# Optimization experiments

Hardware: AMD Instinct MI355X
Metric: run time of the kernel (lower is better)

## Reference

```python
import jax, jax.numpy as jnp
import numpy as np


def setup_inputs() -> dict:
    key = jax.random.key(0)
    k1, k2, k3 = jax.random.split(key, 3)
    B, S, D = 2, 2048, 1024
    N_COMPRESS, RANK = 64, 64
    x = jax.random.normal(k1, (B, S, D), dtype=jnp.float32)
    router_w = jax.random.normal(k2, (N_COMPRESS, D), dtype=jnp.float32) * (1.0 / np.sqrt(D))
    # compress neurons (orthogonal-init in torch; gaussian scaled is fine for a numeric baseline)
    neurons = jax.random.normal(k3, (N_COMPRESS, D, RANK), dtype=jnp.float32) * (1.0 / np.sqrt(D))
    return {"x": x, "router_w": router_w, "neurons": neurons}


TOP_K = 2


def reference(x, router_w, neurons):
    # x: [B,S,D], router_w: [N,D], neurons: [N,D,R]
    B, S, D = x.shape
    R = neurons.shape[-1]
    scores = jnp.einsum('bsd,nd->bsn', x, router_w)            # [B,S,N]
    topk_scores, topk_idx = jax.lax.top_k(scores, TOP_K)       # [B,S,K]
    topk_weights = jax.nn.softmax(topk_scores, axis=-1)        # [B,S,K]
    output = jnp.zeros((B, S, R), dtype=x.dtype)
    for i in range(TOP_K):  # small fixed loop, mirrors original slot-wise combine
        idx = topk_idx[:, :, i]                                # [B,S]
        sel = neurons[idx]                                     # [B,S,D,R] gather
        proj = jnp.einsum('bsd,bsdr->bsr', x, sel)             # per-token matvec
        output = output + topk_weights[:, :, i:i + 1] * proj
    return output, topk_idx, topk_weights
```

## Files before the change

### kernel.cpp

```cpp
#include <hip/hip_runtime.h>
#include <hip/hip_bf16.h>


typedef unsigned short u16;
typedef unsigned int u32;
typedef __attribute__((ext_vector_type(8))) short short8;
typedef __attribute__((ext_vector_type(4))) float f32x4;

__device__ __forceinline__ float bf2f(u16 u) {
    u32 v = ((u32)u) << 16; float f; __builtin_memcpy(&f, &v, 4); return f;
}
__device__ __forceinline__ u16 f2bf(float f) {
    u32 u; __builtin_memcpy(&u, &f, 4);
    u32 r = u + 0x7fff + ((u >> 16) & 1);
    return (u16)(r >> 16);
}
__device__ __forceinline__ u32 pack2(float a, float b) {
    return ((u32)f2bf(b) << 16) | (u32)f2bf(a);
}

#define T_TOKENS 4096
#define DDIM 1024
#define NEXP 64
#define RDIM 64
#define LCAP 1024
#define OUT_IDX_OFF 262144
#define OUT_W_OFF 270336

struct LdBF {
    const u16* p;
    __device__ __forceinline__ float4 ld4(size_t i) const {
        ushort4 v = *(const ushort4*)(p + i);
        return make_float4(bf2f(v.x), bf2f(v.y), bf2f(v.z), bf2f(v.w));
    }
    __device__ __forceinline__ float ld1(size_t i) const { return bf2f(p[i]); }
};
struct LdF32 {
    const float* p;
    __device__ __forceinline__ float4 ld4(size_t i) const { return *(const float4*)(p + i); }
    __device__ __forceinline__ float ld1(size_t i) const { return p[i]; }
};

__device__ __forceinline__ int detect_f32(const u16* x, int* lds_cnt) {
    if (threadIdx.x == 0) *lds_cnt = 0;
    __syncthreads();
    if (threadIdx.x < 256) {
        unsigned e = (x[threadIdx.x] >> 7) & 0xFF;
        if (e >= 0x68 && e <= 0x88) atomicAdd(lds_cnt, 1);
    }
    __syncthreads();
    int f = (*lds_cnt < 200) ? 1 : 0;
    __syncthreads();
    return f;
}

template <class LD>
__device__ __forceinline__ void score_body(LD xld, LD rwld,
                                           float* xs , float* wt ,
                                           float* sc , float* Sb) {
    const int tid = threadIdx.x;
    const int g = blockIdx.x >> 1;
    const int kh = blockIdx.x & 1;
    const size_t t0 = (size_t)g * 8;
    const int kbase = kh * 512;
    const int wv = tid >> 6;
    const int lane = tid & 63;
    const int tg = lane & 1;
    const int eg = (lane >> 1) & 7;
    const int kql = (lane >> 4) & 3;
    const int dd = 4 * kql + 16 * wv;
    const int kc0 = blockIdx.x & 7;

    const int sm = tid >> 4;
    const int sd4 = (tid & 15) * 4;

    float acc[4][8];
#pragma unroll
    for (int mi = 0; mi < 4; ++mi)
#pragma unroll
        for (int ei = 0; ei < 8; ++ei) acc[mi][ei] = 0.f;

    float4 px;
    if (tid < 128) px = xld.ld4((t0 + sm) * DDIM + kbase + kc0 * 64 + sd4);
    float4 pw[4];
#pragma unroll
    for (int h = 0; h < 4; ++h) {
        int i4 = tid + h * 256;
        pw[h] = rwld.ld4((size_t)(i4 >> 4) * DDIM + kbase + kc0 * 64 + (i4 & 15) * 4);
    }

    for (int i = 0; i < 8; ++i) {
        if (i > 0) __syncthreads();
        if (tid < 128) *(float4*)&xs[sm * 68 + sd4] = px;
#pragma unroll
        for (int h = 0; h < 4; ++h) {
            int i4 = tid + h * 256;
            *(float4*)&wt[(i4 >> 4) * 68 + (i4 & 15) * 4] = pw[h];
        }
        __syncthreads();

        if (i < 7) {
            int kn = kbase + ((i + 1 + kc0) & 7) * 64;
            if (tid < 128) px = xld.ld4((t0 + sm) * DDIM + kn + sd4);
#pragma unroll
            for (int h = 0; h < 4; ++h) {
                int i4 = tid + h * 256;
                pw[h] = rwld.ld4((size_t)(i4 >> 4) * DDIM + kn + (i4 & 15) * 4);
            }
        }

        float4 xv[4], wv4[8];
#pragma unroll
        for (int mi = 0; mi < 4; ++mi)
            xv[mi] = *(const float4*)&xs[(tg + 2 * mi) * 68 + dd];
#pragma unroll
        for (int ei = 0; ei < 8; ++ei)
            wv4[ei] = *(const float4*)&wt[(eg + 8 * ei) * 68 + dd];
#pragma unroll
        for (int mi = 0; mi < 4; ++mi)
#pragma unroll
            for (int ei = 0; ei < 8; ++ei)
                acc[mi][ei] += xv[mi].x * wv4[ei].x + xv[mi].y * wv4[ei].y +
                               xv[mi].z * wv4[ei].z + xv[mi].w * wv4[ei].w;
    }

#pragma unroll
    for (int mi = 0; mi < 4; ++mi)
#pragma unroll
        for (int ei = 0; ei < 8; ++ei) {
            float v = acc[mi][ei];
            v += __shfl_xor(v, 16, 64);
            v += __shfl_xor(v, 32, 64);
            acc[mi][ei] = v;
        }
    __syncthreads();

    for (int w = 0; w < 4; ++w) {
        if (wv == w && kql == 0) {
#pragma unroll
            for (int mi = 0; mi < 4; ++mi)
#pragma unroll
                for (int ei = 0; ei < 8; ++ei) {
                    int idx = (tg + 2 * mi) * 65 + eg + 8 * ei;
                    sc[idx] = (w == 0) ? acc[mi][ei] : sc[idx] + acc[mi][ei];
                }
        }
        __syncthreads();
    }

    if (tid < 128) {
        int t = tid >> 4, e4 = (tid & 15) * 4;
        const float* s = &sc[t * 65 + e4];
        float4 v = make_float4(s[0], s[1], s[2], s[3]);
        *(float4*)&Sb[((size_t)kh * T_TOKENS + t0 + t) * 64 + e4] = v;
    }
}

__global__ __launch_bounds__(256, 4) void score_part(const void* x, const void* rw,
                                                     float* Sb) {
    __shared__ float xs[8 * 68];
    __shared__ float wt[64 * 68];
    __shared__ float sc[8 * 65];
    __shared__ int dc;
    int f = detect_f32((const u16*)x, &dc);
    if (f)
        score_body(LdF32{(const float*)x}, LdF32{(const float*)rw}, xs, wt, sc, Sb);
    else
        score_body(LdBF{(const u16*)x}, LdBF{(const u16*)rw}, xs, wt, sc, Sb);
}

__global__ __launch_bounds__(64) void topk_softmax(const float* Sb, float* out,
                                                   float* wsW, int* wsCnt,
                                                   int* wsList) {
    int t = blockIdx.x * 64 + threadIdx.x;
    const float* s0 = Sb + (size_t)t * 64;
    const float* s1 = Sb + ((size_t)T_TOKENS + t) * 64;
    float best = -1e30f, secv = -1e30f;
    int bi = 0, si = 0;
    for (int j = 0; j < NEXP; j += 4) {
        float4 a = *(const float4*)(s0 + j);
        float4 b = *(const float4*)(s1 + j);
        float v0 = a.x + b.x, v1 = a.y + b.y, v2 = a.z + b.z, v3 = a.w + b.w;
        if (v0 > best) { secv = best; si = bi; best = v0; bi = j; }
        else if (v0 > secv) { secv = v0; si = j; }
        if (v1 > best) { secv = best; si = bi; best = v1; bi = j + 1; }
        else if (v1 > secv) { secv = v1; si = j + 1; }
        if (v2 > best) { secv = best; si = bi; best = v2; bi = j + 2; }
        else if (v2 > secv) { secv = v2; si = j + 2; }
        if (v3 > best) { secv = best; si = bi; best = v3; bi = j + 3; }
        else if (v3 > secv) { secv = v3; si = j + 3; }
    }
    float w0 = 1.0f / (1.0f + expf(secv - best));
    float w1 = 1.0f - w0;
    out[OUT_IDX_OFF + (size_t)t * 2 + 0] = (float)bi;
    out[OUT_IDX_OFF + (size_t)t * 2 + 1] = (float)si;
    out[OUT_W_OFF + (size_t)t * 2 + 0] = w0;
    out[OUT_W_OFF + (size_t)t * 2 + 1] = w1;
    wsW[t * 2 + 0] = w0;
    wsW[t * 2 + 1] = w1;
    int p0 = atomicAdd(&wsCnt[bi], 1);
    if (p0 < LCAP) wsList[bi * LCAP + p0] = t * 2 + 0;
    int p1 = atomicAdd(&wsCnt[si], 1);
    if (p1 < LCAP) wsList[si * LCAP + p1] = t * 2 + 1;
}

template <class LD>
__device__ __forceinline__ void egemm_body(LD xld, LD nld,
                                           const int* wsCnt, const int* wsList,
                                           float* P,
                                           u16* Ab , u16* Bb ,
                                           int* eL ) {
    const int tid = threadIdx.x;
    const int e = blockIdx.x >> 3;
    const int oct = blockIdx.x & 7;
    const int cntE = min(wsCnt[e], LCAP);
    if (cntE <= 0) return;
    const int wv = tid >> 6;
    const int lane = tid & 63;
    const int l15 = lane & 15, quad = lane >> 4;
    const size_t nbase = (size_t)e * (DDIM * RDIM);
    const int k0 = oct * 128;

    for (int j = tid; j < cntE; j += 256) eL[j] = wsList[e * LCAP + j];

    {
        const int rq = tid & 15;
        const int kpB = tid >> 4;
        u32* bb = (u32*)Bb;
#pragma unroll
        for (int h = 0; h < 4; ++h) {
            int kp = kpB + h * 16;
            float4 g0 = nld.ld4(nbase + (size_t)(k0 + 2 * kp) * RDIM + rq * 4);
            float4 g1 = nld.ld4(nbase + (size_t)(k0 + 2 * kp + 1) * RDIM + rq * 4);
            bb[(rq * 4 + 0) * 68 + kp] = pack2(g0.x, g1.x);
            bb[(rq * 4 + 1) * 68 + kp] = pack2(g0.y, g1.y);
            bb[(rq * 4 + 2) * 68 + kp] = pack2(g0.z, g1.z);
            bb[(rq * 4 + 3) * 68 + kp] = pack2(g0.w, g1.w);
        }
    }
    __syncthreads();

    const int rowA = tid >> 4;
    const int kqA = tid & 15;
    const int ntiles = (cntE + 15) >> 4;

    float4 c0, c1, n0, n1;
    {
        int t2r = eL[min(rowA, cntE - 1)];
        size_t xrow = (size_t)(t2r >> 1) * DDIM + k0;
        c0 = xld.ld4(xrow + kqA * 8);
        c1 = xld.ld4(xrow + kqA * 8 + 4);
    }
    n0 = c0; n1 = c1;
    if (ntiles > 1) {
        int t2r = eL[min(16 + rowA, cntE - 1)];
        size_t xrow = (size_t)(t2r >> 1) * DDIM + k0;
        n0 = xld.ld4(xrow + kqA * 8);
        n1 = xld.ld4(xrow + kqA * 8 + 4);
    }

    for (int ti = 0; ti < ntiles; ++ti) {
        const int base = ti * 16;
        const int valid = min(16, cntE - base);
        if (ti > 0) __syncthreads();
        {
            uint4 w;
            w.x = pack2(c0.x, c0.y);
            w.y = pack2(c0.z, c0.w);
            w.z = pack2(c1.x, c1.y);
            w.w = pack2(c1.z, c1.w);
            *(uint4*)&((u32*)Ab)[rowA * 68 + kqA * 4] = w;
        }
        __syncthreads();
        if (ti + 2 < ntiles) {
            int t2r = eL[min(base + 32 + rowA, cntE - 1)];
            size_t xrow = (size_t)(t2r >> 1) * DDIM + k0;
            c0 = xld.ld4(xrow + kqA * 8);
            c1 = xld.ld4(xrow + kqA * 8 + 4);
        }

        f32x4 acc = {0.f, 0.f, 0.f, 0.f};
#pragma unroll
        for (int ko = 0; ko < 4; ++ko) {
            int kofs = ko * 32 + quad * 8;
            short8 bfr = *(const short8*)&Bb[(16 * wv + l15) * 136 + kofs];
            short8 af = *(const short8*)&Ab[l15 * 136 + kofs];
            acc = __builtin_amdgcn_mfma_f32_16x16x32_bf16(af, bfr, acc, 0, 0, 0);
        }

#pragma unroll
        for (int reg = 0; reg < 4; ++reg) {
            int m = quad * 4 + reg;
            if (m < valid) {
                int t2 = eL[base + m];
                P[(size_t)t2 * 512 + oct * 64 + 16 * wv + l15] = acc[reg];
            }
        }

        float4 s0 = c0, s1 = c1;
        c0 = n0; c1 = n1;
        n0 = s0; n1 = s1;
    }
}

__global__ __launch_bounds__(256, 2) void expert_gemm(const void* x, const void* neurons,
                                                      const int* wsCnt, const int* wsList,
                                                      float* P) {
    __shared__ u16 Ab[16 * 136];
    __shared__ u16 Bb[64 * 136];
    __shared__ int eL[LCAP];
    __shared__ int dc;
    int f = detect_f32((const u16*)x, &dc);
    if (f)
        egemm_body(LdF32{(const float*)x}, LdF32{(const float*)neurons}, wsCnt, wsList, P, Ab, Bb, eL);
    else
        egemm_body(LdBF{(const u16*)x}, LdBF{(const u16*)neurons}, wsCnt, wsList, P, Ab, Bb, eL);
}

__global__ __launch_bounds__(256) void combine(const float* P, const float* wsW,
                                               float* out) {
    int i = blockIdx.x * 256 + threadIdx.x;
    int t = i >> 6, r = i & 63;
    const float* p0 = P + (size_t)(2 * t) * 512 + r;
    const float* p1 = P + (size_t)(2 * t + 1) * 512 + r;
    float s0 = 0.f, s1 = 0.f;
#pragma unroll
    for (int o = 0; o < 8; ++o) {
        s0 += p0[o * 64];
        s1 += p1[o * 64];
    }
    out[i] = wsW[2 * t] * s0 + wsW[2 * t + 1] * s1;
}

extern "C" void kernel_launch(void* const* d_in, const int* in_sizes, int n_in,
                              void* d_out, int out_size, void* d_ws, size_t ws_size,
                              hipStream_t stream) {
    const void* x = d_in[0];
    const void* rw = d_in[1];
    const void* neurons = d_in[2];
    float* out = (float*)d_out;

    char* wsc = (char*)d_ws;
    float* wsW = (float*)wsc;
    int* wsCnt = (int*)(wsc + 32 * 1024);
    int* wsList = (int*)(wsc + 32 * 1024 + 256);
    float* Sb = (float*)(wsc + (1 << 20));
    float* P = (float*)(wsc + (4 << 20));

    hipMemsetAsync(wsCnt, 0, 256, stream);
    score_part<<<1024, 256, 0, stream>>>(x, rw, Sb);
    topk_softmax<<<64, 64, 0, stream>>>(Sb, out, wsW, wsCnt, wsList);
    expert_gemm<<<512, 256, 0, stream>>>(x, neurons, wsCnt, wsList, P);
    combine<<<1024, 256, 0, stream>>>(P, wsW, out);
}
```

Measured before the change: 123.9 us.

## Keep router-weight K-slice resident in LDS and stream token tiles through it

The score kernel now splits K into four quarters per block and loads that 64x256 router-weight slice into LDS once. It then loops over eight 8-token tiles, prefetching the next tile of x, instead of reloading the full router tile for every 8 tokens. This removes the redundant router-weight global traffic, but the grid drops from 1024 to 256 blocks at one block per SM, and LDS use grows to about 80 KB. Partial scores now come in four K-quarters, so topk_softmax sums four buffers and the workspace offset for P moves to make room.

```diff
diff --git a/kernel.cpp b/kernel.cpp
--- a/kernel.cpp
+++ b/kernel.cpp
@@ -56,117 +56,130 @@
 
 template <class LD>
 __device__ __forceinline__ void score_body(LD xld, LD rwld,
-                                           float* xs , float* wt ,
-                                           float* sc , float* Sb) {
+                                           float* wt4 , float* xs4 ,
+                                           float* scW , float* Sb) {
     const int tid = threadIdx.x;
-    const int g = blockIdx.x >> 1;
-    const int kh = blockIdx.x & 1;
-    const size_t t0 = (size_t)g * 8;
-    const int kbase = kh * 512;
+    const int q = blockIdx.x & 3;
+    const int p = blockIdx.x >> 2;
+    const size_t tp0 = (size_t)p * 64;
+    const int kq0 = q * 256;
     const int wv = tid >> 6;
     const int lane = tid & 63;
     const int tg = lane & 1;
     const int eg = (lane >> 1) & 7;
     const int kql = (lane >> 4) & 3;
     const int dd = 4 * kql + 16 * wv;
-    const int kc0 = blockIdx.x & 7;
-
-    const int sm = tid >> 4;
-    const int sd4 = (tid & 15) * 4;
-
-    float acc[4][8];
-#pragma unroll
-    for (int mi = 0; mi < 4; ++mi)
-#pragma unroll
-        for (int ei = 0; ei < 8; ++ei) acc[mi][ei] = 0.f;
-
-    float4 px;
-    if (tid < 128) px = xld.ld4((t0 + sm) * DDIM + kbase + kc0 * 64 + sd4);
-    float4 pw[4];
-#pragma unroll
-    for (int h = 0; h < 4; ++h) {
-        int i4 = tid + h * 256;
-        pw[h] = rwld.ld4((size_t)(i4 >> 4) * DDIM + kbase + kc0 * 64 + (i4 & 15) * 4);
-    }
-
-    for (int i = 0; i < 8; ++i) {
-        if (i > 0) __syncthreads();
-        if (tid < 128) *(float4*)&xs[sm * 68 + sd4] = px;
-#pragma unroll
-        for (int h = 0; h < 4; ++h) {
-            int i4 = tid + h * 256;
-            *(float4*)&wt[(i4 >> 4) * 68 + (i4 & 15) * 4] = pw[h];
+
+    {
+        float4 pA[4], pB[4];
+#define RW_LOAD(c, P4)                                                            \
+        _Pragma("unroll")                                                         \
+        for (int h = 0; h < 4; ++h) {                                             \
+            int i4 = tid + h * 256;                                               \
+            P4[h] = rwld.ld4((size_t)(i4 >> 4) * DDIM + kq0 + (c) * 64 + (i4 & 15) * 4); \
+        }
+#define RW_WRITE(c, P4)                                                           \
+        _Pragma("unroll")                                                         \
+        for (int h = 0; h < 4; ++h) {                                             \
+            int i4 = tid + h * 256;                                               \
+            *(float4*)&wt4[(c) * 4352 + (i4 >> 4) * 68 + (i4 & 15) * 4] = P4[h];  \
+        }
+        RW_LOAD(0, pA); RW_LOAD(1, pB);
+        RW_WRITE(0, pA); RW_LOAD(2, pA);
+        RW_WRITE(1, pB); RW_LOAD(3, pB);
+        RW_WRITE(2, pA);
+        RW_WRITE(3, pB);
+#undef RW_LOAD
+#undef RW_WRITE
+    }
+
+    const int tk0 = tid >> 6, f40 = tid & 63;
+    float4 px0, px1;
+    px0 = xld.ld4((tp0 + tk0) * DDIM + kq0 + f40 * 4);
+    px1 = xld.ld4((tp0 + tk0 + 4) * DDIM + kq0 + f40 * 4);
+
+    for (int it = 0; it < 8; ++it) {
+        {
+            int c0 = f40 >> 4, pos = (f40 & 15) * 4;
+            *(float4*)&xs4[c0 * 544 + tk0 * 68 + pos] = px0;
+            *(float4*)&xs4[c0 * 544 + (tk0 + 4) * 68 + pos] = px1;
         }
         __syncthreads();
 
-        if (i < 7) {
-            int kn = kbase + ((i + 1 + kc0) & 7) * 64;
-            if (tid < 128) px = xld.ld4((t0 + sm) * DDIM + kn + sd4);
-#pragma unroll
-            for (int h = 0; h < 4; ++h) {
-                int i4 = tid + h * 256;
-                pw[h] = rwld.ld4((size_t)(i4 >> 4) * DDIM + kn + (i4 & 15) * 4);
+        if (it < 7) {
+            size_t tn = tp0 + (it + 1) * 8;
+            px0 = xld.ld4((tn + tk0) * DDIM + kq0 + f40 * 4);
+            px1 = xld.ld4((tn + tk0 + 4) * DDIM + kq0 + f40 * 4);
+        }
+
+        float acc[4][8];
+#pragma unroll
+        for (int mi = 0; mi < 4; ++mi)
+#pragma unroll
+            for (int ei = 0; ei < 8; ++ei) acc[mi][ei] = 0.f;
+
+#pragma unroll
+        for (int c = 0; c < 4; ++c) {
+            float4 xv[4], wv4[8];
+#pragma unroll
+            for (int mi = 0; mi < 4; ++mi)
+                xv[mi] = *(const float4*)&xs4[c * 544 + (tg + 2 * mi) * 68 + dd];
+#pragma unroll
+            for (int ei = 0; ei < 8; ++ei)
+                wv4[ei] = *(const float4*)&wt4[c * 4352 + (eg + 8 * ei) * 68 + dd];
+#pragma unroll
+            for (int mi = 0; mi < 4; ++mi)
+#pragma unroll
+                for (int ei = 0; ei < 8; ++ei)
+                    acc[mi][ei] += xv[mi].x * wv4[ei].x + xv[mi].y * wv4[ei].y +
+                                   xv[mi].z * wv4[ei].z + xv[mi].w * wv4[ei].w;
+        }
+
+#pragma unroll
+        for (int mi = 0; mi < 4; ++mi)
+#pragma unroll
+            for (int ei = 0; ei < 8; ++ei) {
+                float v = acc[mi][ei];
+                v += __shfl_xor(v, 16, 64);
+                v += __shfl_xor(v, 32, 64);
+                acc[mi][ei] = v;
             }
-        }
-
-        float4 xv[4], wv4[8];
-#pragma unroll
-        for (int mi = 0; mi < 4; ++mi)
-            xv[mi] = *(const float4*)&xs[(tg + 2 * mi) * 68 + dd];
-#pragma unroll
-        for (int ei = 0; ei < 8; ++ei)
-            wv4[ei] = *(const float4*)&wt[(eg + 8 * ei) * 68 + dd];
-#pragma unroll
-        for (int mi = 0; mi < 4; ++mi)
-#pragma unroll
-            for (int ei = 0; ei < 8; ++ei)
-                acc[mi][ei] += xv[mi].x * wv4[ei].x + xv[mi].y * wv4[ei].y +
-                               xv[mi].z * wv4[ei].z + xv[mi].w * wv4[ei].w;
-    }
-
-#pragma unroll
-    for (int mi = 0; mi < 4; ++mi)
-#pragma unroll
-        for (int ei = 0; ei < 8; ++ei) {
-            float v = acc[mi][ei];
-            v += __shfl_xor(v, 16, 64);
-            v += __shfl_xor(v, 32, 64);
-            acc[mi][ei] = v;
-        }
-    __syncthreads();
-
-    for (int w = 0; w < 4; ++w) {
-        if (wv == w && kql == 0) {
+        __syncthreads();
+
+        if (kql == 0) {
 #pragma unroll
             for (int mi = 0; mi < 4; ++mi)
 #pragma unroll
-                for (int ei = 0; ei < 8; ++ei) {
-                    int idx = (tg + 2 * mi) * 65 + eg + 8 * ei;
-                    sc[idx] = (w == 0) ? acc[mi][ei] : sc[idx] + acc[mi][ei];
-                }
+                for (int ei = 0; ei < 8; ++ei)
+                    scW[wv * 520 + (tg + 2 * mi) * 65 + eg + 8 * ei] = acc[mi][ei];
         }
         __syncthreads();
-    }
-
-    if (tid < 128) {
-        int t = tid >> 4, e4 = (tid & 15) * 4;
-        const float* s = &sc[t * 65 + e4];
-        float4 v = make_float4(s[0], s[1], s[2], s[3]);
-        *(float4*)&Sb[((size_t)kh * T_TOKENS + t0 + t) * 64 + e4] = v;
-    }
-}
-
-__global__ __launch_bounds__(256, 4) void score_part(const void* x, const void* rw,
+
+        {
+            size_t tg0 = tp0 + it * 8;
+#pragma unroll
+            for (int hh = 0; hh < 2; ++hh) {
+                int cell = tid + hh * 256;
+                int t = cell >> 6, e = cell & 63;
+                float v = scW[0 * 520 + t * 65 + e] + scW[1 * 520 + t * 65 + e] +
+                          scW[2 * 520 + t * 65 + e] + scW[3 * 520 + t * 65 + e];
+                Sb[((size_t)q * T_TOKENS + tg0 + t) * 64 + e] = v;
+            }
+        }
+    }
+}
+
+__global__ __launch_bounds__(256, 1) void score_part(const void* x, const void* rw,
                                                      float* Sb) {
-    __shared__ float xs[8 * 68];
-    __shared__ float wt[64 * 68];
-    __shared__ float sc[8 * 65];
+    __shared__ float wt4[4 * 64 * 68];
+    __shared__ float xs4[4 * 8 * 68];
+    __shared__ float scW[4 * 8 * 65];
     __shared__ int dc;
     int f = detect_f32((const u16*)x, &dc);
     if (f)
-        score_body(LdF32{(const float*)x}, LdF32{(const float*)rw}, xs, wt, sc, Sb);
+        score_body(LdF32{(const float*)x}, LdF32{(const float*)rw}, wt4, xs4, scW, Sb);
     else
-        score_body(LdBF{(const u16*)x}, LdBF{(const u16*)rw}, xs, wt, sc, Sb);
+        score_body(LdBF{(const u16*)x}, LdBF{(const u16*)rw}, wt4, xs4, scW, Sb);
 }
 
 __global__ __launch_bounds__(64) void topk_softmax(const float* Sb, float* out,
@@ -174,13 +187,20 @@
                                                    int* wsList) {
     int t = blockIdx.x * 64 + threadIdx.x;
     const float* s0 = Sb + (size_t)t * 64;
-    const float* s1 = Sb + ((size_t)T_TOKENS + t) * 64;
+    const float* s1 = s0 + (size_t)T_TOKENS * 64;
+    const float* s2 = s1 + (size_t)T_TOKENS * 64;
+    const float* s3 = s2 + (size_t)T_TOKENS * 64;
     float best = -1e30f, secv = -1e30f;
     int bi = 0, si = 0;
     for (int j = 0; j < NEXP; j += 4) {
         float4 a = *(const float4*)(s0 + j);
         float4 b = *(const float4*)(s1 + j);
-        float v0 = a.x + b.x, v1 = a.y + b.y, v2 = a.z + b.z, v3 = a.w + b.w;
+        float4 c = *(const float4*)(s2 + j);
+        float4 d = *(const float4*)(s3 + j);
+        float v0 = ((a.x + b.x) + c.x) + d.x;
+        float v1 = ((a.y + b.y) + c.y) + d.y;
+        float v2 = ((a.z + b.z) + c.z) + d.z;
+        float v3 = ((a.w + b.w) + c.w) + d.w;
         if (v0 > best) { secv = best; si = bi; best = v0; bi = j; }
         else if (v0 > secv) { secv = v0; si = j; }
         if (v1 > best) { secv = best; si = bi; best = v1; bi = j + 1; }
@@ -345,10 +365,10 @@
     int* wsCnt = (int*)(wsc + 32 * 1024);
     int* wsList = (int*)(wsc + 32 * 1024 + 256);
     float* Sb = (float*)(wsc + (1 << 20));
-    float* P = (float*)(wsc + (4 << 20));
+    float* P = (float*)(wsc + (8 << 20));
 
     hipMemsetAsync(wsCnt, 0, 256, stream);
-    score_part<<<1024, 256, 0, stream>>>(x, rw, Sb);
+    score_part<<<256, 256, 0, stream>>>(x, rw, Sb);
     topk_softmax<<<64, 64, 0, stream>>>(Sb, out, wsW, wsCnt, wsList);
     expert_gemm<<<512, 256, 0, stream>>>(x, neurons, wsCnt, wsList, P);
     combine<<<1024, 256, 0, stream>>>(P, wsW, out);
```

After: 136.2 us. +9.9%, slower.
